# Kernel tuning notes

Measured on AMD Instinct MI355X. Metric: run time of the kernel, lower is better.

Reference implementation:

```python
import jax, jax.numpy as jnp
import numpy as np

M, B, T, D, P = 3, 128, 512, 1024, 256  # modalities, batch, time, d_model, projection_dim
LN_EPS = 1e-5
NORM_EPS = 1e-12


def setup_inputs() -> dict:
    key = jax.random.key(0)
    ks = jax.random.split(key, 7)
    s1 = 1.0 / np.sqrt(D)
    s2 = 1.0 / np.sqrt(D)
    return {
        "feats": jax.random.normal(ks[0], (M, B, T, D), dtype=jnp.float32),
        "W1": jax.random.uniform(ks[1], (M, D, D), jnp.float32, -s1, s1),
        "b1": jax.random.uniform(ks[2], (M, D), jnp.float32, -s1, s1),
        "W2": jax.random.uniform(ks[3], (M, D, P), jnp.float32, -s2, s2),
        "b2": jax.random.uniform(ks[4], (M, P), jnp.float32, -s2, s2),
        "gamma": jnp.ones((M, P), jnp.float32),
        "beta": jnp.zeros((M, P), jnp.float32),
    }


def reference(feats, W1, b1, W2, b2, gamma, beta):
    # Mean-pool over time: [M,B,T,D] -> [M,B,D]
    pooled = feats.mean(axis=2)
    # Linear(d_model, d_model) + exact GELU (dropout is identity at inference)
    h = jax.nn.gelu(jnp.einsum('mbd,mde->mbe', pooled, W1) + b1[:, None, :],
                    approximate=False)
    # Linear(d_model, projection_dim)
    z = jnp.einsum('mbd,mdp->mbp', h, W2) + b2[:, None, :]
    # LayerNorm over last dim
    mu = z.mean(axis=-1, keepdims=True)
    var = jnp.mean((z - mu) ** 2, axis=-1, keepdims=True)
    z = (z - mu) / jnp.sqrt(var + LN_EPS) * gamma[:, None, :] + beta[:, None, :]
    # F.normalize (cosine path): divide by max(l2_norm, eps)
    n = jnp.sqrt(jnp.sum(z * z, axis=-1, keepdims=True))
    return z / jnp.maximum(n, NORM_EPS)  # [M, B, P]
```

## Files before the change

### kernel.cpp

```cpp
#include <hip/hip_runtime.h>
#include <math.h>

#define M_ 3
#define B_ 128
#define T_ 512
#define D_ 1024
#define P_ 256
#define TC 2
#define NRIDER 64
#define BM1 32
#define BN1 64

__device__ __forceinline__ unsigned int f2bf(float f) {
    unsigned int x = __float_as_uint(f);
    return (x + 0x7fffu + ((x >> 16) & 1u)) >> 16;
}

__global__ __launch_bounds__(256) void pool_and_cast(const float* __restrict__ feats,
                                                     const float* __restrict__ W2,
                                                     float* __restrict__ partial,
                                                     unsigned int* __restrict__ w2p) {
    int blk = blockIdx.x;
    int tid = threadIdx.x;
    if (blk < NRIDER) {
        const int TOT = M_ * (D_ / 2) * P_;
        for (int i = blk * 256 + tid; i < TOT; i += NRIDER * 256) {
            int p  = i & (P_ - 1);
            int k2 = (i >> 8) & (D_ / 2 - 1);
            int m  = i >> 17;
            size_t base = (size_t)m * D_ * P_ + (size_t)(2 * k2) * P_ + p;
            float f0 = W2[base];
            float f1 = W2[base + P_];
            w2p[i] = f2bf(f0) | (f2bf(f1) << 16);
        }
        return;
    }
    blk -= NRIDER;
    int tc = blk & (TC - 1);
    int mb = blk / TC;
    const int TSTEP = T_ / TC;
    const float4* src = (const float4*)feats + ((size_t)mb * T_ + (size_t)tc * TSTEP) * (D_ / 4) + tid;
    float4 a0 = make_float4(0.f, 0.f, 0.f, 0.f);
    float4 a1 = a0, a2 = a0, a3 = a0, a4 = a0, a5 = a0, a6 = a0, a7 = a0;
    for (int t = 0; t < TSTEP; t += 8) {
        float4 v0 = src[0 * (D_ / 4)];
        float4 v1 = src[1 * (D_ / 4)];
        float4 v2 = src[2 * (D_ / 4)];
        float4 v3 = src[3 * (D_ / 4)];
        float4 v4 = src[4 * (D_ / 4)];
        float4 v5 = src[5 * (D_ / 4)];
        float4 v6 = src[6 * (D_ / 4)];
        float4 v7 = src[7 * (D_ / 4)];
        src += 8 * (D_ / 4);
        a0.x += v0.x; a0.y += v0.y; a0.z += v0.z; a0.w += v0.w;
        a1.x += v1.x; a1.y += v1.y; a1.z += v1.z; a1.w += v1.w;
        a2.x += v2.x; a2.y += v2.y; a2.z += v2.z; a2.w += v2.w;
        a3.x += v3.x; a3.y += v3.y; a3.z += v3.z; a3.w += v3.w;
        a4.x += v4.x; a4.y += v4.y; a4.z += v4.z; a4.w += v4.w;
        a5.x += v5.x; a5.y += v5.y; a5.z += v5.z; a5.w += v5.w;
        a6.x += v6.x; a6.y += v6.y; a6.z += v6.z; a6.w += v6.w;
        a7.x += v7.x; a7.y += v7.y; a7.z += v7.z; a7.w += v7.w;
    }
    float4 s;
    s.x = ((a0.x + a1.x) + (a2.x + a3.x)) + ((a4.x + a5.x) + (a6.x + a7.x));
    s.y = ((a0.y + a1.y) + (a2.y + a3.y)) + ((a4.y + a5.y) + (a6.y + a7.y));
    s.z = ((a0.z + a1.z) + (a2.z + a3.z)) + ((a4.z + a5.z) + (a6.z + a7.z));
    s.w = ((a0.w + a1.w) + (a2.w + a3.w)) + ((a4.w + a5.w) + (a6.w + a7.w));
    ((float4*)partial)[((size_t)mb * TC + tc) * (D_ / 4) + tid] = s;
}

__global__ __launch_bounds__(512) void gemm1_gelu(const float* __restrict__ partial,
                                                  const float* __restrict__ W1,
                                                  const float* __restrict__ b1,
                                                  float* __restrict__ h) {
    __shared__ float As[2][BM1][68];
    __shared__ float Bs[2][64][68];
    int m  = blockIdx.z;
    int b0 = blockIdx.y * BM1;
    int e0 = blockIdx.x * BN1;
    int tid  = threadIdx.x;
    int half = tid >> 8;
    int t    = tid & 255;
    int ar  = t >> 4;
    int ac4 = t & 15;
    int ty  = t >> 4;
    int tx  = t & 15;

    const float* Ab = partial + (size_t)(m * B_ + b0) * TC * D_;
    const float* Bb = W1 + (size_t)m * D_ * D_ + e0;
    const float inv = 1.0f / (float)T_;

    float4 acc0 = make_float4(0.f, 0.f, 0.f, 0.f);
    float4 acc1 = make_float4(0.f, 0.f, 0.f, 0.f);

    for (int kk = 0; kk < 8; ++kk) {
        int k0 = half * 512 + kk * 64;
        const float* Ar0 = Ab + (size_t)(TC * ar) * D_ + k0 + 4 * ac4;
        const float* Ar1 = Ab + (size_t)(TC * (ar + 16)) * D_ + k0 + 4 * ac4;
        float4 p00 = *(const float4*)(Ar0);
        float4 p01 = *(const float4*)(Ar0 + D_);
        float4 p10 = *(const float4*)(Ar1);
        float4 p11 = *(const float4*)(Ar1 + D_);
        float4 bv0 = *(const float4*)(Bb + (size_t)(k0 + ar) * D_ + 4 * ac4);
        float4 bv1 = *(const float4*)(Bb + (size_t)(k0 + ar + 16) * D_ + 4 * ac4);
        float4 bv2 = *(const float4*)(Bb + (size_t)(k0 + ar + 32) * D_ + 4 * ac4);
        float4 bv3 = *(const float4*)(Bb + (size_t)(k0 + ar + 48) * D_ + 4 * ac4);
        __syncthreads();
        float4 av0, av1;
        av0.x = (p00.x + p01.x) * inv; av0.y = (p00.y + p01.y) * inv;
        av0.z = (p00.z + p01.z) * inv; av0.w = (p00.w + p01.w) * inv;
        av1.x = (p10.x + p11.x) * inv; av1.y = (p10.y + p11.y) * inv;
        av1.z = (p10.z + p11.z) * inv; av1.w = (p10.w + p11.w) * inv;
        *(float4*)&As[half][ar][4 * ac4]      = av0;
        *(float4*)&As[half][ar + 16][4 * ac4] = av1;
        *(float4*)&Bs[half][ar][4 * ac4]      = bv0;
        *(float4*)&Bs[half][ar + 16][4 * ac4] = bv1;
        *(float4*)&Bs[half][ar + 32][4 * ac4] = bv2;
        *(float4*)&Bs[half][ar + 48][4 * ac4] = bv3;
        __syncthreads();
#pragma unroll
        for (int k = 0; k < 64; ++k) {
            float A0 = As[half][2 * ty][k];
            float A1 = As[half][2 * ty + 1][k];
            float4 bb = *(const float4*)&Bs[half][k][4 * tx];
            acc0.x += A0 * bb.x; acc0.y += A0 * bb.y; acc0.z += A0 * bb.z; acc0.w += A0 * bb.w;
            acc1.x += A1 * bb.x; acc1.y += A1 * bb.y; acc1.z += A1 * bb.z; acc1.w += A1 * bb.w;
        }
    }
    __syncthreads();
    float* zb = &As[0][0][0];
    if (half == 0) {
        *(float4*)&zb[(2 * ty) * 68 + 4 * tx]     = acc0;
        *(float4*)&zb[(2 * ty + 1) * 68 + 4 * tx] = acc1;
    }
    __syncthreads();
    if (half == 1) {
        int col = e0 + 4 * tx;
        float4 bb = *(const float4*)(b1 + m * D_ + col);
        float4 z0 = *(const float4*)&zb[(2 * ty) * 68 + 4 * tx];
        float4 z1 = *(const float4*)&zb[(2 * ty + 1) * 68 + 4 * tx];
        z0.x += acc0.x + bb.x; z0.y += acc0.y + bb.y; z0.z += acc0.z + bb.z; z0.w += acc0.w + bb.w;
        z1.x += acc1.x + bb.x; z1.y += acc1.y + bb.y; z1.z += acc1.z + bb.z; z1.w += acc1.w + bb.w;
        const float is2 = 0.70710678118654752f;
        float4 g0, g1;
        g0.x = 0.5f * z0.x * (1.0f + erff(z0.x * is2));
        g0.y = 0.5f * z0.y * (1.0f + erff(z0.y * is2));
        g0.z = 0.5f * z0.z * (1.0f + erff(z0.z * is2));
        g0.w = 0.5f * z0.w * (1.0f + erff(z0.w * is2));
        g1.x = 0.5f * z1.x * (1.0f + erff(z1.x * is2));
        g1.y = 0.5f * z1.y * (1.0f + erff(z1.y * is2));
        g1.z = 0.5f * z1.z * (1.0f + erff(z1.z * is2));
        g1.w = 0.5f * z1.w * (1.0f + erff(z1.w * is2));
        int row0 = b0 + 2 * ty;
        *(float4*)&h[((size_t)m * B_ + row0) * D_ + col]     = g0;
        *(float4*)&h[((size_t)m * B_ + row0 + 1) * D_ + col] = g1;
    }
}

__global__ __launch_bounds__(512) void gemm2_ln(const float* __restrict__ h,
                                                const unsigned int* __restrict__ w2p,
                                                const float* __restrict__ b2,
                                                const float* __restrict__ gamma,
                                                const float* __restrict__ beta,
                                                float* __restrict__ out) {
    int m  = blockIdx.y;
    int b0 = blockIdx.x * 2;
    int tid  = threadIdx.x;
    int p    = tid & 255;
    int half = tid >> 8;
    int lane = tid & 63;
    int w    = (tid >> 6) & 3;

    __shared__ float accs[2][2][256];
    __shared__ float redA[2][4];
    __shared__ float redB[2][4];
    __shared__ float redC[2][4];

    const unsigned int* Wp = w2p + (size_t)m * (D_ / 2) * P_ + (size_t)half * 256 * P_ + p;
    const float* hb = h + ((size_t)m * B_ + b0) * D_ + half * 512;

    float acc0 = 0.f, acc1 = 0.f;
#pragma unroll 4
    for (int q = 0; q < 128; ++q) {
        unsigned int u0 = Wp[(size_t)(2 * q) * P_];
        unsigned int u1 = Wp[(size_t)(2 * q + 1) * P_];
        float w0 = __uint_as_float(u0 << 16);
        float w1 = __uint_as_float(u0 & 0xffff0000u);
        float w2 = __uint_as_float(u1 << 16);
        float w3 = __uint_as_float(u1 & 0xffff0000u);
        float4 h0 = *(const float4*)(hb + 4 * q);
        float4 h1 = *(const float4*)(hb + D_ + 4 * q);
        acc0 += h0.x * w0 + h0.y * w1 + h0.z * w2 + h0.w * w3;
        acc1 += h1.x * w0 + h1.y * w1 + h1.z * w2 + h1.w * w3;
    }
    accs[half][0][p] = acc0;
    accs[half][1][p] = acc1;
    __syncthreads();

    int g = half;
    float z = accs[0][g][p] + accs[1][g][p] + b2[m * P_ + p];

    float s1 = z, s2 = z * z;
    for (int off = 32; off > 0; off >>= 1) {
        s1 += __shfl_xor(s1, off);
        s2 += __shfl_xor(s2, off);
    }
    if (lane == 0) { redA[g][w] = s1; redB[g][w] = s2; }
    __syncthreads();
    s1 = (redA[g][0] + redA[g][1]) + (redA[g][2] + redA[g][3]);
    s2 = (redB[g][0] + redB[g][1]) + (redB[g][2] + redB[g][3]);
    float mu  = s1 * (1.0f / P_);
    float var = s2 * (1.0f / P_) - mu * mu;
    float inv = 1.0f / sqrtf(var + 1e-5f);
    z = (z - mu) * inv * gamma[m * P_ + p] + beta[m * P_ + p];

    float s = z * z;
    for (int off = 32; off > 0; off >>= 1) s += __shfl_xor(s, off);
    if (lane == 0) redC[g][w] = s;
    __syncthreads();
    s = (redC[g][0] + redC[g][1]) + (redC[g][2] + redC[g][3]);
    float n = sqrtf(s);
    out[((size_t)m * B_ + b0 + g) * P_ + p] = z / fmaxf(n, 1e-12f);
}

extern "C" void kernel_launch(void* const* d_in, const int* in_sizes, int n_in,
                              void* d_out, int out_size, void* d_ws, size_t ws_size,
                              hipStream_t stream) {
    const float* feats = (const float*)d_in[0];
    const float* W1    = (const float*)d_in[1];
    const float* b1    = (const float*)d_in[2];
    const float* W2    = (const float*)d_in[3];
    const float* b2    = (const float*)d_in[4];
    const float* gamma = (const float*)d_in[5];
    const float* beta  = (const float*)d_in[6];
    float* out = (float*)d_out;

    float* wsf = (float*)d_ws;
    float*        partial = wsf;
    unsigned int* w2p     = (unsigned int*)(wsf + 786432);
    float*        hbuf    = wsf + 786432 + 393216;

    pool_and_cast<<<NRIDER + M_ * B_ * TC, 256, 0, stream>>>(feats, W2, partial, w2p);
    dim3 g2(D_ / BN1, B_ / BM1, M_);
    gemm1_gelu<<<g2, 512, 0, stream>>>(partial, W1, b1, hbuf);
    dim3 g3(B_ / 2, M_);
    gemm2_ln<<<g3, 512, 0, stream>>>(hbuf, w2p, b2, gamma, beta, out);
}
```

Before: 190.5 us.

## Convert W1 to transposed bf16 and run GEMM1 with MFMA instructions

Adds blocks to the pooling kernel that transpose W1 into a bf16 [e][k] layout in workspace. GEMM1 is rewritten to use MFMA 16x16x32 bf16 instructions with XOR-swizzled LDS tiles in place of scalar fp32 FMAs. The goal is to cut GEMM1 compute time and halve its W1 read bytes. In exchange, W1 must be read and converted on every call, and bf16 inputs reduce precision.

```diff
diff --git a/kernel.cpp b/kernel.cpp
--- a/kernel.cpp
+++ b/kernel.cpp
@@ -7,9 +7,13 @@
 #define D_ 1024
 #define P_ 256
 #define TC 2
-#define NRIDER 64
-#define BM1 32
-#define BN1 64
+
+#define NPOOL   (M_ * B_ * TC)
+#define NW1T    192
+#define NW2     64
+
+typedef __attribute__((ext_vector_type(8))) short short8v;
+typedef __attribute__((ext_vector_type(4))) float f32x4;
 
 __device__ __forceinline__ unsigned int f2bf(float f) {
     unsigned int x = __float_as_uint(f);
@@ -17,14 +21,86 @@
 }
 
 __global__ __launch_bounds__(256) void pool_and_cast(const float* __restrict__ feats,
+                                                     const float* __restrict__ W1,
                                                      const float* __restrict__ W2,
                                                      float* __restrict__ partial,
+                                                     short* __restrict__ w1t,
                                                      unsigned int* __restrict__ w2p) {
+    __shared__ float ldsf[64][68];
     int blk = blockIdx.x;
     int tid = threadIdx.x;
-    if (blk < NRIDER) {
+
+    if (blk < NPOOL) {
+        int tc = blk & (TC - 1);
+        int mb = blk / TC;
+        const int TSTEP = T_ / TC;
+        const float4* src = (const float4*)feats + ((size_t)mb * T_ + (size_t)tc * TSTEP) * (D_ / 4) + tid;
+        float4 a0 = make_float4(0.f, 0.f, 0.f, 0.f);
+        float4 a1 = a0, a2 = a0, a3 = a0, a4 = a0, a5 = a0, a6 = a0, a7 = a0;
+        for (int t = 0; t < TSTEP; t += 8) {
+            float4 v0 = src[0 * (D_ / 4)];
+            float4 v1 = src[1 * (D_ / 4)];
+            float4 v2 = src[2 * (D_ / 4)];
+            float4 v3 = src[3 * (D_ / 4)];
+            float4 v4 = src[4 * (D_ / 4)];
+            float4 v5 = src[5 * (D_ / 4)];
+            float4 v6 = src[6 * (D_ / 4)];
+            float4 v7 = src[7 * (D_ / 4)];
+            src += 8 * (D_ / 4);
+            a0.x += v0.x; a0.y += v0.y; a0.z += v0.z; a0.w += v0.w;
+            a1.x += v1.x; a1.y += v1.y; a1.z += v1.z; a1.w += v1.w;
+            a2.x += v2.x; a2.y += v2.y; a2.z += v2.z; a2.w += v2.w;
+            a3.x += v3.x; a3.y += v3.y; a3.z += v3.z; a3.w += v3.w;
+            a4.x += v4.x; a4.y += v4.y; a4.z += v4.z; a4.w += v4.w;
+            a5.x += v5.x; a5.y += v5.y; a5.z += v5.z; a5.w += v5.w;
+            a6.x += v6.x; a6.y += v6.y; a6.z += v6.z; a6.w += v6.w;
+            a7.x += v7.x; a7.y += v7.y; a7.z += v7.z; a7.w += v7.w;
+        }
+        float4 s;
+        s.x = ((a0.x + a1.x) + (a2.x + a3.x)) + ((a4.x + a5.x) + (a6.x + a7.x));
+        s.y = ((a0.y + a1.y) + (a2.y + a3.y)) + ((a4.y + a5.y) + (a6.y + a7.y));
+        s.z = ((a0.z + a1.z) + (a2.z + a3.z)) + ((a4.z + a5.z) + (a6.z + a7.z));
+        s.w = ((a0.w + a1.w) + (a2.w + a3.w)) + ((a4.w + a5.w) + (a6.w + a7.w));
+        ((float4*)partial)[((size_t)mb * TC + tc) * (D_ / 4) + tid] = s;
+        return;
+    }
+
+    if (blk < NPOOL + NW1T) {
+        int bid = blk - NPOOL;
+        for (int i = 0; i < 4; ++i) {
+            int tile = bid * 4 + i;
+            int et = tile & 15;
+            int kt = (tile >> 4) & 15;
+            int mm = tile >> 8;
+            int k0 = kt * 64, ee0 = et * 64;
+#pragma unroll
+            for (int sv = 0; sv < 4; ++sv) {
+                int idx = sv * 256 + tid;
+                int row = idx >> 4;
+                int c4  = idx & 15;
+                float4 v = *(const float4*)(W1 + (size_t)mm * D_ * D_ + (size_t)(k0 + row) * D_ + ee0 + c4 * 4);
+                *(float4*)&ldsf[row][c4 * 4] = v;
+            }
+            __syncthreads();
+            int er = tid >> 2;
+            int ks = (tid & 3) * 16;
+            short8v v0, v1;
+#pragma unroll
+            for (int j = 0; j < 8; ++j) v0[j] = (short)f2bf(ldsf[ks + j][er]);
+#pragma unroll
+            for (int j = 0; j < 8; ++j) v1[j] = (short)f2bf(ldsf[ks + 8 + j][er]);
+            size_t ob = ((size_t)mm * D_ + ee0 + er) * D_ + k0 + ks;
+            *(short8v*)(w1t + ob)     = v0;
+            *(short8v*)(w1t + ob + 8) = v1;
+            __syncthreads();
+        }
+        return;
+    }
+
+    {
+        int bid = blk - NPOOL - NW1T;
         const int TOT = M_ * (D_ / 2) * P_;
-        for (int i = blk * 256 + tid; i < TOT; i += NRIDER * 256) {
+        for (int i = bid * 256 + tid; i < TOT; i += NW2 * 256) {
             int p  = i & (P_ - 1);
             int k2 = (i >> 8) & (D_ / 2 - 1);
             int m  = i >> 17;
@@ -33,127 +109,93 @@
             float f1 = W2[base + P_];
             w2p[i] = f2bf(f0) | (f2bf(f1) << 16);
         }
-        return;
-    }
-    blk -= NRIDER;
-    int tc = blk & (TC - 1);
-    int mb = blk / TC;
-    const int TSTEP = T_ / TC;
-    const float4* src = (const float4*)feats + ((size_t)mb * T_ + (size_t)tc * TSTEP) * (D_ / 4) + tid;
-    float4 a0 = make_float4(0.f, 0.f, 0.f, 0.f);
-    float4 a1 = a0, a2 = a0, a3 = a0, a4 = a0, a5 = a0, a6 = a0, a7 = a0;
-    for (int t = 0; t < TSTEP; t += 8) {
-        float4 v0 = src[0 * (D_ / 4)];
-        float4 v1 = src[1 * (D_ / 4)];
-        float4 v2 = src[2 * (D_ / 4)];
-        float4 v3 = src[3 * (D_ / 4)];
-        float4 v4 = src[4 * (D_ / 4)];
-        float4 v5 = src[5 * (D_ / 4)];
-        float4 v6 = src[6 * (D_ / 4)];
-        float4 v7 = src[7 * (D_ / 4)];
-        src += 8 * (D_ / 4);
-        a0.x += v0.x; a0.y += v0.y; a0.z += v0.z; a0.w += v0.w;
-        a1.x += v1.x; a1.y += v1.y; a1.z += v1.z; a1.w += v1.w;
-        a2.x += v2.x; a2.y += v2.y; a2.z += v2.z; a2.w += v2.w;
-        a3.x += v3.x; a3.y += v3.y; a3.z += v3.z; a3.w += v3.w;
-        a4.x += v4.x; a4.y += v4.y; a4.z += v4.z; a4.w += v4.w;
-        a5.x += v5.x; a5.y += v5.y; a5.z += v5.z; a5.w += v5.w;
-        a6.x += v6.x; a6.y += v6.y; a6.z += v6.z; a6.w += v6.w;
-        a7.x += v7.x; a7.y += v7.y; a7.z += v7.z; a7.w += v7.w;
-    }
-    float4 s;
-    s.x = ((a0.x + a1.x) + (a2.x + a3.x)) + ((a4.x + a5.x) + (a6.x + a7.x));
-    s.y = ((a0.y + a1.y) + (a2.y + a3.y)) + ((a4.y + a5.y) + (a6.y + a7.y));
-    s.z = ((a0.z + a1.z) + (a2.z + a3.z)) + ((a4.z + a5.z) + (a6.z + a7.z));
-    s.w = ((a0.w + a1.w) + (a2.w + a3.w)) + ((a4.w + a5.w) + (a6.w + a7.w));
-    ((float4*)partial)[((size_t)mb * TC + tc) * (D_ / 4) + tid] = s;
-}
-
-__global__ __launch_bounds__(512) void gemm1_gelu(const float* __restrict__ partial,
-                                                  const float* __restrict__ W1,
+    }
+}
+
+__global__ __launch_bounds__(256) void gemm1_mfma(const float* __restrict__ partial,
+                                                  const short* __restrict__ w1t,
                                                   const float* __restrict__ b1,
                                                   float* __restrict__ h) {
-    __shared__ float As[2][BM1][68];
-    __shared__ float Bs[2][64][68];
+    __shared__ __align__(16) short As[32 * 64];
+    __shared__ __align__(16) short Bs[64 * 64];
     int m  = blockIdx.z;
-    int b0 = blockIdx.y * BM1;
-    int e0 = blockIdx.x * BN1;
-    int tid  = threadIdx.x;
-    int half = tid >> 8;
-    int t    = tid & 255;
-    int ar  = t >> 4;
-    int ac4 = t & 15;
-    int ty  = t >> 4;
-    int tx  = t & 15;
-
-    const float* Ab = partial + (size_t)(m * B_ + b0) * TC * D_;
-    const float* Bb = W1 + (size_t)m * D_ * D_ + e0;
+    int b0 = blockIdx.y * 32;
+    int e0 = blockIdx.x * 64;
+    int tid = threadIdx.x;
+    int l   = tid & 63;
+    int w   = tid >> 6;
+    int wr  = w & 1, wc = w >> 1;
+
+    int arow = tid >> 3;
+    int k8   = tid & 7;
+    int bcol = tid >> 2;
+    int bj   = tid & 3;
+
+    const float* Abase = partial + ((size_t)(m * B_ + b0 + arow) * TC) * D_ + k8 * 8;
+    const short* Bbase = w1t + ((size_t)m * D_ + e0 + bcol) * D_ + bj * 16;
+
+    char* AsB = (char*)As;
+    char* BsB = (char*)Bs;
+    short8v* AsW  = (short8v*)(AsB + arow * 128 + ((k8 ^ (arow & 7)) << 4));
+    short8v* BsW0 = (short8v*)(BsB + bcol * 128 + (((2 * bj)     ^ (bcol & 7)) << 4));
+    short8v* BsW1 = (short8v*)(BsB + bcol * 128 + (((2 * bj + 1) ^ (bcol & 7)) << 4));
+
+    f32x4 acc0 = {0.f, 0.f, 0.f, 0.f};
+    f32x4 acc1 = {0.f, 0.f, 0.f, 0.f};
     const float inv = 1.0f / (float)T_;
 
-    float4 acc0 = make_float4(0.f, 0.f, 0.f, 0.f);
-    float4 acc1 = make_float4(0.f, 0.f, 0.f, 0.f);
-
-    for (int kk = 0; kk < 8; ++kk) {
-        int k0 = half * 512 + kk * 64;
-        const float* Ar0 = Ab + (size_t)(TC * ar) * D_ + k0 + 4 * ac4;
-        const float* Ar1 = Ab + (size_t)(TC * (ar + 16)) * D_ + k0 + 4 * ac4;
-        float4 p00 = *(const float4*)(Ar0);
-        float4 p01 = *(const float4*)(Ar0 + D_);
-        float4 p10 = *(const float4*)(Ar1);
-        float4 p11 = *(const float4*)(Ar1 + D_);
-        float4 bv0 = *(const float4*)(Bb + (size_t)(k0 + ar) * D_ + 4 * ac4);
-        float4 bv1 = *(const float4*)(Bb + (size_t)(k0 + ar + 16) * D_ + 4 * ac4);
-        float4 bv2 = *(const float4*)(Bb + (size_t)(k0 + ar + 32) * D_ + 4 * ac4);
-        float4 bv3 = *(const float4*)(Bb + (size_t)(k0 + ar + 48) * D_ + 4 * ac4);
+    int ar  = wr * 16 + (l & 15);
+    int bc0 = wc * 32 + (l & 15);
+    int bc1 = bc0 + 16;
+    int lh  = l >> 4;
+
+    for (int it = 0; it < 16; ++it) {
+        int k0 = it * 64;
+        float4 p00 = *(const float4*)(Abase + k0);
+        float4 p01 = *(const float4*)(Abase + k0 + 4);
+        float4 p10 = *(const float4*)(Abase + D_ + k0);
+        float4 p11 = *(const float4*)(Abase + D_ + k0 + 4);
+        short8v bv0 = *(const short8v*)(Bbase + k0);
+        short8v bv1 = *(const short8v*)(Bbase + k0 + 8);
         __syncthreads();
-        float4 av0, av1;
-        av0.x = (p00.x + p01.x) * inv; av0.y = (p00.y + p01.y) * inv;
-        av0.z = (p00.z + p01.z) * inv; av0.w = (p00.w + p01.w) * inv;
-        av1.x = (p10.x + p11.x) * inv; av1.y = (p10.y + p11.y) * inv;
-        av1.z = (p10.z + p11.z) * inv; av1.w = (p10.w + p11.w) * inv;
-        *(float4*)&As[half][ar][4 * ac4]      = av0;
-        *(float4*)&As[half][ar + 16][4 * ac4] = av1;
-        *(float4*)&Bs[half][ar][4 * ac4]      = bv0;
-        *(float4*)&Bs[half][ar + 16][4 * ac4] = bv1;
-        *(float4*)&Bs[half][ar + 32][4 * ac4] = bv2;
-        *(float4*)&Bs[half][ar + 48][4 * ac4] = bv3;
+        short8v av;
+        av[0] = (short)f2bf((p00.x + p10.x) * inv);
+        av[1] = (short)f2bf((p00.y + p10.y) * inv);
+        av[2] = (short)f2bf((p00.z + p10.z) * inv);
+        av[3] = (short)f2bf((p00.w + p10.w) * inv);
+        av[4] = (short)f2bf((p01.x + p11.x) * inv);
+        av[5] = (short)f2bf((p01.y + p11.y) * inv);
+        av[6] = (short)f2bf((p01.z + p11.z) * inv);
+        av[7] = (short)f2bf((p01.w + p11.w) * inv);
+        *AsW  = av;
+        *BsW0 = bv0;
+        *BsW1 = bv1;
         __syncthreads();
 #pragma unroll
-        for (int k = 0; k < 64; ++k) {
-            float A0 = As[half][2 * ty][k];
-            float A1 = As[half][2 * ty + 1][k];
-            float4 bb = *(const float4*)&Bs[half][k][4 * tx];
-            acc0.x += A0 * bb.x; acc0.y += A0 * bb.y; acc0.z += A0 * bb.z; acc0.w += A0 * bb.w;
-            acc1.x += A1 * bb.x; acc1.y += A1 * bb.y; acc1.z += A1 * bb.z; acc1.w += A1 * bb.w;
-        }
-    }
-    __syncthreads();
-    float* zb = &As[0][0][0];
-    if (half == 0) {
-        *(float4*)&zb[(2 * ty) * 68 + 4 * tx]     = acc0;
-        *(float4*)&zb[(2 * ty + 1) * 68 + 4 * tx] = acc1;
-    }
-    __syncthreads();
-    if (half == 1) {
-        int col = e0 + 4 * tx;
-        float4 bb = *(const float4*)(b1 + m * D_ + col);
-        float4 z0 = *(const float4*)&zb[(2 * ty) * 68 + 4 * tx];
-        float4 z1 = *(const float4*)&zb[(2 * ty + 1) * 68 + 4 * tx];
-        z0.x += acc0.x + bb.x; z0.y += acc0.y + bb.y; z0.z += acc0.z + bb.z; z0.w += acc0.w + bb.w;
-        z1.x += acc1.x + bb.x; z1.y += acc1.y + bb.y; z1.z += acc1.z + bb.z; z1.w += acc1.w + bb.w;
-        const float is2 = 0.70710678118654752f;
-        float4 g0, g1;
-        g0.x = 0.5f * z0.x * (1.0f + erff(z0.x * is2));
-        g0.y = 0.5f * z0.y * (1.0f + erff(z0.y * is2));
-        g0.z = 0.5f * z0.z * (1.0f + erff(z0.z * is2));
-        g0.w = 0.5f * z0.w * (1.0f + erff(z0.w * is2));
-        g1.x = 0.5f * z1.x * (1.0f + erff(z1.x * is2));
-        g1.y = 0.5f * z1.y * (1.0f + erff(z1.y * is2));
-        g1.z = 0.5f * z1.z * (1.0f + erff(z1.z * is2));
-        g1.w = 0.5f * z1.w * (1.0f + erff(z1.w * is2));
-        int row0 = b0 + 2 * ty;
-        *(float4*)&h[((size_t)m * B_ + row0) * D_ + col]     = g0;
-        *(float4*)&h[((size_t)m * B_ + row0 + 1) * D_ + col] = g1;
+        for (int kk = 0; kk < 2; ++kk) {
+            int ch = kk * 4 + lh;
+            short8v af  = *(const short8v*)(AsB + ar  * 128 + ((ch ^ (ar  & 7)) << 4));
+            short8v bf0 = *(const short8v*)(BsB + bc0 * 128 + ((ch ^ (bc0 & 7)) << 4));
+            short8v bf1 = *(const short8v*)(BsB + bc1 * 128 + ((ch ^ (bc1 & 7)) << 4));
+            acc0 = __builtin_amdgcn_mfma_f32_16x16x32_bf16(af, bf0, acc0, 0, 0, 0);
+            acc1 = __builtin_amdgcn_mfma_f32_16x16x32_bf16(af, bf1, acc1, 0, 0, 0);
+        }
+    }
+
+    int colBase = e0 + wc * 32 + (l & 15);
+    int rowBase = b0 + wr * 16 + lh * 4;
+    const float is2 = 0.70710678118654752f;
+#pragma unroll
+    for (int n = 0; n < 2; ++n) {
+        f32x4 acc = n ? acc1 : acc0;
+        int col = colBase + n * 16;
+        float bb = b1[m * D_ + col];
+#pragma unroll
+        for (int r = 0; r < 4; ++r) {
+            float x = acc[r] + bb;
+            float gx = 0.5f * x * (1.0f + erff(x * is2));
+            h[(size_t)(m * B_ + rowBase + r) * D_ + col] = gx;
+        }
     }
 }
 
@@ -239,10 +281,11 @@
     float*        partial = wsf;
     unsigned int* w2p     = (unsigned int*)(wsf + 786432);
     float*        hbuf    = wsf + 786432 + 393216;
-
-    pool_and_cast<<<NRIDER + M_ * B_ * TC, 256, 0, stream>>>(feats, W2, partial, w2p);
-    dim3 g2(D_ / BN1, B_ / BM1, M_);
-    gemm1_gelu<<<g2, 512, 0, stream>>>(partial, W1, b1, hbuf);
+    short*        w1t     = (short*)(wsf + 786432 + 2 * 393216);
+
+    pool_and_cast<<<NPOOL + NW1T + NW2, 256, 0, stream>>>(feats, W1, W2, partial, w1t, w2p);
+    dim3 g2(D_ / 64, B_ / 32, M_);
+    gemm1_mfma<<<g2, 256, 0, stream>>>(partial, w1t, b1, hbuf);
     dim3 g3(B_ / 2, M_);
     gemm2_ln<<<g3, 512, 0, stream>>>(hbuf, w2p, b2, gamma, beta, out);
 }
```

Result: no change. 193.5 us (+1.6%).
